# Performance work log

Measured on AMD Instinct MI355X. Metric: run time of the kernel, lower is better.

Reference implementation:

```python
import jax, jax.numpy as jnp
import numpy as np

# scNET (vae_flag=False, cd=False, eval mode): genes x cells matrix;
# PPI graph over 3000 genes, KNN graph over 4096 cells.
N_GENES, N_CELLS = 3000, 4096          # col_dim, row_dim
INTER_R, EMBD_R = 512, 128             # gene (rows) encoder dims
INTER_C, EMBD_C = 1024, 256            # cell (cols) encoder dims
N_LAYERS = 2
KNN_E, PPI_E = 65536, 262144
SCALE_PARAM = 3.0                      # TransformerConvReducrLayer scale_param


def setup_inputs() -> dict:
    key = jax.random.key(0)
    ks = iter(jax.random.split(key, 64))
    def lin(shape):
        fan_in = shape[-2]
        return jax.random.normal(next(ks), shape, jnp.float32) / np.sqrt(fan_in)
    inp = {}
    inp["x"] = jax.random.normal(next(ks), (N_GENES, N_CELLS), jnp.float32)
    inp["knn_ei"] = jax.random.randint(next(ks), (2, KNN_E), 0, N_CELLS)
    inp["ppi_ei"] = jax.random.randint(next(ks), (2, PPI_E), 0, N_GENES)
    inp["rl_W"] = lin((N_CELLS, N_CELLS)); inp["rl_b"] = jnp.zeros((N_CELLS,), jnp.float32)
    inp["rs_Wl"] = lin((N_LAYERS, N_CELLS, N_CELLS)); inp["rs_Wr"] = lin((N_LAYERS, N_CELLS, N_CELLS))
    inp["rs_b"] = jnp.zeros((N_LAYERS, N_CELLS), jnp.float32)
    inp["cs_Wl"] = lin((N_LAYERS, N_GENES, N_GENES)); inp["cs_Wr"] = lin((N_LAYERS, N_GENES, N_GENES))
    inp["cs_b"] = jnp.zeros((N_LAYERS, N_GENES), jnp.float32)
    inp["rg_W"] = lin((N_CELLS, INTER_R)); inp["rg_b"] = jnp.zeros((INTER_R,), jnp.float32)
    for nm in ("rq", "rk", "rv", "rsk"):
        inp[nm + "_W"] = lin((INTER_R, EMBD_R)); inp[nm + "_b"] = jnp.zeros((EMBD_R,), jnp.float32)
    inp["cg_W"] = lin((N_GENES, INTER_C)); inp["cg_b"] = jnp.zeros((INTER_C,), jnp.float32)
    for nm in ("cq", "ck", "cv", "csk"):
        inp[nm + "_W"] = lin((INTER_C, EMBD_C)); inp[nm + "_b"] = jnp.zeros((EMBD_C,), jnp.float32)
    inp["d1_W"] = lin((EMBD_C, INTER_C)); inp["d1_b"] = jnp.zeros((INTER_C,), jnp.float32)
    inp["d2_W"] = lin((INTER_C, INTER_C)); inp["d2_b"] = jnp.zeros((INTER_C,), jnp.float32)
    inp["d3_W"] = lin((INTER_C, N_GENES)); inp["d3_b"] = jnp.zeros((N_GENES,), jnp.float32)
    return inp


def sage_conv(x, ei, Wl, Wr, b):
    # PyG SAGEConv (mean aggr, root weight): lin_l(mean_{j->i} x_j) + lin_r(x_i) + b
    n = x.shape[0]
    src, dst = ei[0], ei[1]
    s = jax.ops.segment_sum(x[src], dst, num_segments=n)
    cnt = jax.ops.segment_sum(jnp.ones((ei.shape[1],), x.dtype), dst, num_segments=n)
    agg = s / jnp.maximum(cnt, 1.0)[:, None]
    return agg @ Wl + x @ Wr + b


def gcn_conv(x, ei, W, b):
    # PyG GCNConv: self loops + symmetric D^-1/2 (A+I) D^-1/2 normalization
    n = x.shape[0]
    idx = jnp.arange(n)
    src = jnp.concatenate([ei[0], idx])
    dst = jnp.concatenate([ei[1], idx])
    deg = jax.ops.segment_sum(jnp.ones((src.shape[0],), x.dtype), dst, num_segments=n)
    dinv = jax.lax.rsqrt(jnp.maximum(deg, 1.0))
    h = x @ W
    msg = h[src] * (dinv[src] * dinv[dst])[:, None]
    return jax.ops.segment_sum(msg, dst, num_segments=n) + b


def transformer_conv(x, ei, Wq, bq, Wk, bk, Wv, bv, Ws, bs, scale_param):
    # PyG TransformerConv (heads=1). scale_param=None -> per-destination segment
    # softmax; otherwise scNET's globally sigmoid-normalized attention
    # (TransformerConvReducrLayer.message): global mean/std standardize -> sigmoid.
    n = x.shape[0]
    d = Wq.shape[1]
    src, dst = ei[0], ei[1]
    q = x @ Wq + bq
    k = x @ Wk + bk
    v = x @ Wv + bv
    alpha = (q[dst] * k[src]).sum(-1) / jnp.sqrt(jnp.asarray(d, x.dtype))  # [E]
    if scale_param is None:
        m = jax.ops.segment_max(alpha, dst, num_segments=n)
        e = jnp.exp(alpha - m[dst])
        z = jax.ops.segment_sum(e, dst, num_segments=n)
        alpha = e / (z[dst] + 1e-16)
    else:
        alpha = (alpha - alpha.mean()) / ((1.0 / scale_param) * jnp.std(alpha, ddof=1))
        alpha = jax.nn.sigmoid(alpha)
    out = jax.ops.segment_sum(v[src] * alpha[:, None], dst, num_segments=n)
    return out + (x @ Ws + bs)  # root skip (lin_skip)


def reference(x, knn_ei, ppi_ei, rl_W, rl_b, rs_Wl, rs_Wr, rs_b, cs_Wl, cs_Wr, cs_b,
              rg_W, rg_b, rq_W, rq_b, rk_W, rk_b, rv_W, rv_b, rsk_W, rsk_b,
              cg_W, cg_b, cq_W, cq_b, ck_W, ck_b, cv_W, cv_b, csk_W, csk_b,
              d1_W, d1_b, d2_W, d2_b, d3_W, d3_b):
    # MutaelEncoder: row linear then alternating col/row SAGE layers (dropout=id in eval)
    h = x @ rl_W + rl_b                                   # [G, C]
    for i in range(N_LAYERS):
        h = jax.nn.leaky_relu(sage_conv(h.T, knn_ei, cs_Wl[i], cs_Wr[i], cs_b[i]), 0.01).T
        h = jax.nn.leaky_relu(sage_conv(h, ppi_ei, rs_Wl[i], rs_Wr[i], rs_b[i]), 0.01)
    # rows (gene) DimEncoder: GCN -> LeakyReLU -> TransformerConv (softmax attention)
    r = jax.nn.leaky_relu(gcn_conv(h, ppi_ei, rg_W, rg_b), 0.01)
    row_embed = transformer_conv(r, ppi_ei, rq_W, rq_b, rk_W, rk_b, rv_W, rv_b, rsk_W, rsk_b, None)
    # cols (cell) DimEncoder (reducer): GCN -> LeakyReLU -> sigmoid-normalized attention
    c = jax.nn.leaky_relu(gcn_conv(h.T, knn_ei, cg_W, cg_b), 0.01)
    col_embed = transformer_conv(c, knn_ei, cq_W, cq_b, ck_W, ck_b, cv_W, cv_b, csk_W, csk_b, SCALE_PARAM)
    # FatureDecoder (cd=False): 3-layer MLP with ReLU (dropout=id in eval)
    d = jax.nn.relu(col_embed @ d1_W + d1_b)
    d = jax.nn.relu(d @ d2_W + d2_b)
    recon = d @ d3_W + d3_b                               # [C_cells, G]
    return row_embed, col_embed, recon
```

## Files before the change

### kernel.cpp

```cpp
#include <hip/hip_runtime.h>
#include <math.h>

#define N_GENES 3000
#define N_CELLS 4096
#define GPAD    3072
#define INTER_R 512
#define EMBD_R  128
#define INTER_C 1024
#define EMBD_C  256
#define KNN_E   65536
#define PPI_E   262144

typedef unsigned short u16;
typedef __bf16 bf16x8 __attribute__((ext_vector_type(8)));
typedef float f32x4 __attribute__((ext_vector_type(4)));

__device__ __forceinline__ float b2f(u16 u) {
  union { unsigned i; float f; } x; x.i = ((unsigned)u) << 16; return x.f;
}
__device__ __forceinline__ u16 f2b(float f) {
  union { float f; unsigned i; } x; x.f = f;
  unsigned r = (x.i + 0x7FFFu + ((x.i >> 16) & 1u)) >> 16;
  return (u16)r;
}

typedef const void __attribute__((address_space(1))) gvoid;
typedef void __attribute__((address_space(3))) svoid;
__device__ __forceinline__ void gload16(const void* g, void* l) {
  __builtin_amdgcn_global_load_lds((gvoid*)g, (svoid*)l, 16, 0, 0);
}

template <int OUTF32, int MF>
__global__ __launch_bounds__(512, 1) void mgemm8_k(
    const u16* __restrict__ A, int lda, const u16* __restrict__ BT, int ldb,
    const float* __restrict__ bias, int biasRow, void* __restrict__ Cv, int ldc,
    int M, int N, int K, int accum, int act, int nbx) {
  constexpr int MFH = MF / 2;
  constexpr int TM = MF * 32;
  constexpr int ABYTES = TM * 64;
  constexpr int BBYTES = 16384;
  constexpr int BUFB = 2 * ABYTES + 2 * BBYTES;
  __shared__ char S[2 * BUFB];
  const int t = threadIdx.x;
  const int wid = t >> 6;
  const int l = t & 63;
  const int wm = wid >> 2, wn = wid & 3;
  const int fr = l & 15, hi = l >> 4;

  int nwg = gridDim.x, bid = blockIdx.x;
  int q = nwg >> 3, r = nwg & 7, xcd = bid & 7, seq = bid >> 3;
  int sid = (xcd < r ? xcd * (q + 1) : r * (q + 1) + (xcd - r) * q) + seq;
  int by = sid / nbx, bx = sid - by * nbx;
  const int row0 = by * TM, col0 = bx * 256;

  f32x4 acc[MF][4];
#pragma unroll
  for (int i = 0; i < MF; i++)
#pragma unroll
    for (int j = 0; j < 4; j++) acc[i][j] = (f32x4){0.f, 0.f, 0.f, 0.f};

  const int cA1 = t, cA2 = t + 512;
  const int rA1 = cA1 >> 2, rA2 = cA2 >> 2;
  const int gA1 = (cA1 & 3) ^ ((rA1 >> 1) & 3);
  const int gA2 = (cA2 & 3) ^ ((rA2 >> 1) & 3);
  int arow1 = row0 + rA1; arow1 = arow1 < M ? arow1 : M - 1;
  int arow2 = row0 + (rA2 < TM ? rA2 : TM - 1); arow2 = arow2 < M ? arow2 : M - 1;
  const u16* baseA1 = A + (size_t)arow1 * lda + gA1 * 8;
  const u16* baseA2 = A + (size_t)arow2 * lda + gA2 * 8;
  const bool doA2 = (MF == 8) || (t < 256);
  int brow1 = col0 + rA1; brow1 = brow1 < N ? brow1 : N - 1;
  int brow2 = col0 + rA2; brow2 = brow2 < N ? brow2 : N - 1;
  const u16* baseB1 = BT + (size_t)brow1 * ldb + gA1 * 8;
  const u16* baseB2 = BT + (size_t)brow2 * ldb + gA2 * 8;

  auto aoff = [](int buf, int kh) { return buf * BUFB + kh * ABYTES; };
  auto boff = [](int buf, int kh) { return buf * BUFB + 2 * ABYTES + kh * BBYTES; };

  auto stageA = [&](int buf, int kh, int kt) {
    int ko = kt * 64 + kh * 32;
    gload16(baseA1 + ko, S + aoff(buf, kh) + cA1 * 16);
    if (doA2) gload16(baseA2 + ko, S + aoff(buf, kh) + cA2 * 16);
  };
  auto stageB = [&](int buf, int kh, int kt) {
    int ko = kt * 64 + kh * 32;
    gload16(baseB1 + ko, S + boff(buf, kh) + cA1 * 16);
    gload16(baseB2 + ko, S + boff(buf, kh) + cA2 * 16);
  };

  bf16x8 af[MFH], bfr[4];
  auto dsrA = [&](int buf, int kh, int mh) {
#pragma unroll
    for (int i = 0; i < MFH; i++) {
      int row = wm * (MF * 16) + (mh * MFH + i) * 16 + fr;
      af[i] = *(const bf16x8*)(S + aoff(buf, kh) + row * 64 +
                               ((hi ^ ((row >> 1) & 3)) << 4));
    }
  };
  auto dsrB = [&](int buf, int kh) {
#pragma unroll
    for (int i = 0; i < 4; i++) {
      int row = wn * 64 + i * 16 + fr;
      bfr[i] = *(const bf16x8*)(S + boff(buf, kh) + row * 64 +
                                ((hi ^ ((row >> 1) & 3)) << 4));
    }
  };
  auto mma = [&](int mh) {
    __builtin_amdgcn_s_setprio(1);
#pragma unroll
    for (int i = 0; i < MFH; i++)
#pragma unroll
      for (int j = 0; j < 4; j++)
        acc[mh * MFH + i][j] = __builtin_amdgcn_mfma_f32_16x16x32_bf16(
            af[i], bfr[j], acc[mh * MFH + i][j], 0, 0, 0);
    __builtin_amdgcn_s_setprio(0);
  };
  auto vmw = [&]() {
    if (MF == 6 && wid >= 4)
      asm volatile("s_waitcnt vmcnt(4)" ::: "memory");
    else
      asm volatile("s_waitcnt vmcnt(6)" ::: "memory");
  };
  auto barmid = [&]() {
    __builtin_amdgcn_sched_barrier(0);
    __builtin_amdgcn_s_barrier();
    asm volatile("s_waitcnt lgkmcnt(0)" ::: "memory");
    __builtin_amdgcn_sched_barrier(0);
  };
  auto barend = [&]() {
    __builtin_amdgcn_sched_barrier(0);
    __builtin_amdgcn_s_barrier();
    __builtin_amdgcn_sched_barrier(0);
  };

  const int nt = K >> 6;
  stageA(0, 0, 0); stageB(0, 0, 0); stageA(0, 1, 0); stageB(0, 1, 0);
  stageA(1, 0, 1); stageB(1, 0, 1); stageA(1, 1, 1);
  vmw();
  __builtin_amdgcn_sched_barrier(0);
  __builtin_amdgcn_s_barrier();
  __builtin_amdgcn_sched_barrier(0);

  int p = 0;
  for (int kt = 0; kt < nt - 2; kt++, p ^= 1) {
    dsrA(p, 0, 0); dsrB(p, 0);
    stageB(p ^ 1, 1, kt + 1);
    barmid(); mma(0); barend();
    dsrA(p, 0, 1);
    stageA(p, 0, kt + 2);
    barmid(); mma(1); barend();
    dsrA(p, 1, 0); dsrB(p, 1);
    stageB(p, 0, kt + 2);
    barmid(); mma(0); barend();
    dsrA(p, 1, 1);
    stageA(p, 1, kt + 2);
    vmw();
    barmid(); mma(1); barend();
  }
  dsrA(p, 0, 0); dsrB(p, 0);
  stageB(p ^ 1, 1, nt - 1);
  barmid(); mma(0); barend();
  dsrA(p, 0, 1);
  barmid(); mma(1); barend();
  dsrA(p, 1, 0); dsrB(p, 1);
  barmid(); mma(0); barend();
  dsrA(p, 1, 1);
  asm volatile("s_waitcnt vmcnt(0)" ::: "memory");
  barmid(); mma(1); barend();
  p ^= 1;
  dsrA(p, 0, 0); dsrB(p, 0);
  barmid(); mma(0); barend();
  dsrA(p, 0, 1);
  barmid(); mma(1); barend();
  dsrA(p, 1, 0); dsrB(p, 1);
  barmid(); mma(0); barend();
  dsrA(p, 1, 1);
  barmid(); mma(1); barend();

#pragma unroll
  for (int mf = 0; mf < MF; mf++) {
    int mb = row0 + wm * (MF * 16) + mf * 16 + hi * 4;
#pragma unroll
    for (int rr2 = 0; rr2 < 4; rr2++) {
      int m = mb + rr2;
      if (m >= M) continue;
#pragma unroll
      for (int nf = 0; nf < 4; nf++) {
        int n = col0 + wn * 64 + nf * 16 + fr;
        if (n >= N) continue;
        float v = acc[mf][nf][rr2];
        if (bias) v += biasRow ? bias[m] : bias[n];
        if (OUTF32) {
          float* C = (float*)Cv;
          if (accum) v += C[(size_t)m * ldc + n];
          if (act == 1) v = v > 0.f ? v : 0.01f * v;
          else if (act == 2) v = fmaxf(v, 0.f);
          C[(size_t)m * ldc + n] = v;
        } else {
          u16* C = (u16*)Cv;
          if (accum) v += b2f(C[(size_t)m * ldc + n]);
          if (act == 1) v = v > 0.f ? v : 0.01f * v;
          else if (act == 2) v = fmaxf(v, 0.f);
          C[(size_t)m * ldc + n] = f2b(v);
        }
      }
    }
  }
}

template <int OUTF32>
__global__ __launch_bounds__(256) void mgemm_k(
    const u16* __restrict__ A, int lda, const u16* __restrict__ BT, int ldb,
    const float* __restrict__ bias, void* __restrict__ Cv, int ldc,
    int M, int N, int K, int accum, int act, int nbx) {
  __shared__ u16 As[2][64 * 64];
  __shared__ u16 Bs[2][64 * 64];
  const int t = threadIdx.x;
  const int w = t >> 6, l = t & 63;
  const int wr = w >> 1, wc = w & 1;
  const int fr = l & 15, hi = l >> 4;

  int nwg = gridDim.x, bid = blockIdx.x;
  int q = nwg >> 3, r = nwg & 7, xcd = bid & 7, seq = bid >> 3;
  int sid = (xcd < r ? xcd * (q + 1) : r * (q + 1) + (xcd - r) * q) + seq;
  int by = sid / nbx, bx = sid - by * nbx;
  const int row0 = by * 128, col0 = bx * 128;

  f32x4 acc[4][4];
#pragma unroll
  for (int i = 0; i < 4; i++)
#pragma unroll
    for (int j = 0; j < 4; j++) acc[i][j] = (f32x4){0.f, 0.f, 0.f, 0.f};

  const u16* Aad[2]; const u16* Bad[2];
  char* Alds[2]; char* Blds[2];
#pragma unroll
  for (int c = 0; c < 2; c++) {
    int P = (w * 2 + c) * 64 + l;
    int prow = P >> 3, s = P & 7;
    int lr = prow * 2 + (s >> 2);
    int g = (s & 3) ^ (prow & 3);
    int ar = row0 + lr; ar = ar < M ? ar : M - 1;
    int br = col0 + lr; br = br < N ? br : N - 1;
    Aad[c] = A + (size_t)ar * lda + g * 8;
    Bad[c] = BT + (size_t)br * ldb + g * 8;
    Alds[c] = (char*)&As[0][0] + P * 16;
    Blds[c] = (char*)&Bs[0][0] + P * 16;
  }
  const int nt = K >> 5;
  auto stage = [&](int tt, int b) {
    int ko = tt << 5;
#pragma unroll
    for (int c = 0; c < 2; c++) {
      gload16(Aad[c] + ko, Alds[c] + b * 8192);
      gload16(Bad[c] + ko, Blds[c] + b * 8192);
    }
  };
  auto compute = [&](int tt) {
    const u16* Ab = As[tt & 1];
    const u16* Bb = Bs[tt & 1];
    bf16x8 af[4], bfr[4];
#pragma unroll
    for (int mi = 0; mi < 4; mi++) {
      int row = wr * 64 + mi * 16 + fr;
      int pr = row >> 1;
      af[mi] = *(const bf16x8*)&Ab[pr * 64 + ((row & 1) * 4 + (hi ^ (pr & 3))) * 8];
    }
#pragma unroll
    for (int ni = 0; ni < 4; ni++) {
      int row = wc * 64 + ni * 16 + fr;
      int pr = row >> 1;
      bfr[ni] = *(const bf16x8*)&Bb[pr * 64 + ((row & 1) * 4 + (hi ^ (pr & 3))) * 8];
    }
    __builtin_amdgcn_s_setprio(1);
#pragma unroll
    for (int mi = 0; mi < 4; mi++)
#pragma unroll
      for (int ni = 0; ni < 4; ni++)
        acc[mi][ni] = __builtin_amdgcn_mfma_f32_16x16x32_bf16(
            af[mi], bfr[ni], acc[mi][ni], 0, 0, 0);
    __builtin_amdgcn_s_setprio(0);
  };

  stage(0, 0);
  if (nt > 1) stage(1, 1);
  for (int tt = 0; tt < nt - 1; tt++) {
    asm volatile("s_waitcnt vmcnt(4)" ::: "memory");
    __builtin_amdgcn_sched_barrier(0);
    __builtin_amdgcn_s_barrier();
    __builtin_amdgcn_sched_barrier(0);
    compute(tt);
    __builtin_amdgcn_sched_barrier(0);
    __builtin_amdgcn_s_barrier();
    __builtin_amdgcn_sched_barrier(0);
    if (tt + 2 < nt) stage(tt + 2, tt & 1);
  }
  asm volatile("s_waitcnt vmcnt(0)" ::: "memory");
  __builtin_amdgcn_sched_barrier(0);
  __builtin_amdgcn_s_barrier();
  __builtin_amdgcn_sched_barrier(0);
  compute(nt - 1);

#pragma unroll
  for (int mi = 0; mi < 4; mi++) {
    int mb = row0 + wr * 64 + mi * 16 + hi * 4;
#pragma unroll
    for (int rr2 = 0; rr2 < 4; rr2++) {
      int m = mb + rr2;
      if (m >= M) continue;
#pragma unroll
      for (int ni = 0; ni < 4; ni++) {
        int n = col0 + wc * 64 + ni * 16 + fr;
        if (n >= N) continue;
        float v = acc[mi][ni][rr2];
        if (bias) v += bias[n];
        if (OUTF32) {
          float* C = (float*)Cv;
          if (accum) v += C[(size_t)m * ldc + n];
          if (act == 1) v = v > 0.f ? v : 0.01f * v;
          else if (act == 2) v = fmaxf(v, 0.f);
          C[(size_t)m * ldc + n] = v;
        } else {
          u16* C = (u16*)Cv;
          if (accum) v += b2f(C[(size_t)m * ldc + n]);
          if (act == 1) v = v > 0.f ? v : 0.01f * v;
          else if (act == 2) v = fmaxf(v, 0.f);
          C[(size_t)m * ldc + n] = f2b(v);
        }
      }
    }
  }
}

__global__ void cvtw_k(const float* __restrict__ in, int K, int Nw,
                       u16* __restrict__ out, int ldb, int Kpad) {
  __shared__ float tile[32][33];
  int k0 = blockIdx.y * 32, n0 = blockIdx.x * 32;
  int tx = threadIdx.x & 31, ty = threadIdx.x >> 5;
  for (int i = ty; i < 32; i += 8)
    tile[i][tx] = (k0 + i < K && n0 + tx < Nw) ? in[(size_t)(k0 + i) * Nw + n0 + tx] : 0.f;
  __syncthreads();
  for (int i = ty; i < 32; i += 8) {
    int n = n0 + i, k = k0 + tx;
    if (n < Nw && k < Kpad) out[(size_t)n * ldb + k] = f2b(tile[tx][i]);
  }
}

__global__ void tpad_k(const u16* __restrict__ in, int R, int C, int lin,
                       u16* __restrict__ out, int ostride, int Rpad) {
  __shared__ u16 tile[32][33];
  int r0 = blockIdx.y * 32, c0 = blockIdx.x * 32;
  int tx = threadIdx.x & 31, ty = threadIdx.x >> 5;
  for (int i = ty; i < 32; i += 8)
    tile[i][tx] = (r0 + i < R && c0 + tx < C) ? in[(size_t)(r0 + i) * lin + c0 + tx] : (u16)0;
  __syncthreads();
  for (int i = ty; i < 32; i += 8) {
    int c = c0 + i, r = r0 + tx;
    if (c < C && r < Rpad) out[(size_t)c * ostride + r] = tile[tx][i];
  }
}

__global__ void cvtx_k(const float* __restrict__ in, u16* __restrict__ out, int n) {
  int i = (blockIdx.x * 256 + threadIdx.x) * 4;
  if (i >= n) return;
  float4 v = *(const float4*)&in[i];
  uint2 o;
  o.x = (unsigned)f2b(v.x) | ((unsigned)f2b(v.y) << 16);
  o.y = (unsigned)f2b(v.z) | ((unsigned)f2b(v.w) << 16);
  *(uint2*)&out[i] = o;
}

__global__ void catbias_k(const float* b0, const float* b1, const float* b2,
                          const float* b3, int seg, float* out) {
  int i = blockIdx.x * 256 + threadIdx.x;
  if (i >= 4 * seg) return;
  const float* s = i < seg ? b0 : i < 2 * seg ? b1 : i < 3 * seg ? b2 : b3;
  out[i] = s[i & (seg - 1)];
}

__global__ void zero_i32(int* __restrict__ p, int n) {
  int i = blockIdx.x * 256 + threadIdx.x;
  if (i < n) p[i] = 0;
}
__global__ void count_k(const int* __restrict__ dst, int E, int* __restrict__ cnt) {
  int e = blockIdx.x * 256 + threadIdx.x;
  if (e < E) atomicAdd(&cnt[dst[e]], 1);
}
__global__ __launch_bounds__(1024) void scan_k(const int* __restrict__ cnt,
                                               int* __restrict__ rs, int N) {
  __shared__ int sd[1024];
  int t = threadIdx.x;
  int per = (N + 1023) >> 10;
  int base = t * per;
  int loc[4];
  int s = 0;
  for (int u = 0; u < per; u++) {
    int idx = base + u;
    loc[u] = s;
    int v = (idx < N) ? cnt[idx] : 0;
    s += v;
  }
  sd[t] = s;
  __syncthreads();
  for (int off = 1; off < 1024; off <<= 1) {
    int v = (t >= off) ? sd[t - off] : 0;
    __syncthreads();
    sd[t] += v;
    __syncthreads();
  }
  int prev = (t > 0) ? sd[t - 1] : 0;
  for (int u = 0; u < per; u++) {
    int idx = base + u;
    if (idx < N) rs[idx] = prev + loc[u];
  }
  if (t == 0) rs[N] = sd[1023];
}
__global__ void fill_k(const int* __restrict__ src, const int* __restrict__ dst, int E,
                       const int* __restrict__ rs, int* cursor,
                       int* __restrict__ csrc, int* __restrict__ ceid) {
  int e = blockIdx.x * 256 + threadIdx.x;
  if (e >= E) return;
  int d = dst[e];
  int p = atomicAdd(&cursor[d], 1);
  int b = rs[d] + p;
  csrc[b] = src[e];
  ceid[b] = e;
}
__global__ void dinv_k(const int* __restrict__ rs, float* __restrict__ dinv, int N) {
  int i = blockIdx.x * 256 + threadIdx.x;
  if (i < N) dinv[i] = rsqrtf((float)(rs[i + 1] - rs[i] + 1));
}

__global__ void sage_agg_k(const u16* __restrict__ X, int ld, const int* __restrict__ rs,
                           const int* __restrict__ csrc, u16* __restrict__ out, int D) {
  int i = blockIdx.y;
  int j8 = (blockIdx.x * 256 + threadIdx.x) * 8;
  if (j8 >= D) return;
  int s = rs[i], e = rs[i + 1];
  float a[8] = {0, 0, 0, 0, 0, 0, 0, 0};
  for (int p = s; p < e; p++) {
    uint4 v = *(const uint4*)&X[(size_t)csrc[p] * ld + j8];
    a[0] += b2f(v.x & 0xffff); a[1] += b2f(v.x >> 16);
    a[2] += b2f(v.y & 0xffff); a[3] += b2f(v.y >> 16);
    a[4] += b2f(v.z & 0xffff); a[5] += b2f(v.z >> 16);
    a[6] += b2f(v.w & 0xffff); a[7] += b2f(v.w >> 16);
  }
  float inv = 1.f / fmaxf((float)(e - s), 1.f);
  uint4 o;
  o.x = (unsigned)f2b(a[0] * inv) | ((unsigned)f2b(a[1] * inv) << 16);
  o.y = (unsigned)f2b(a[2] * inv) | ((unsigned)f2b(a[3] * inv) << 16);
  o.z = (unsigned)f2b(a[4] * inv) | ((unsigned)f2b(a[5] * inv) << 16);
  o.w = (unsigned)f2b(a[6] * inv) | ((unsigned)f2b(a[7] * inv) << 16);
  *(uint4*)&out[(size_t)i * ld + j8] = o;
}

__global__ void gcn_agg_k(const u16* __restrict__ HW, int ld, const int* __restrict__ rs,
                          const int* __restrict__ csrc, const float* __restrict__ dinv,
                          const float* __restrict__ bias, u16* __restrict__ out, int D) {
  int i = blockIdx.y;
  int j8 = (blockIdx.x * 256 + threadIdx.x) * 8;
  if (j8 >= D) return;
  int s = rs[i], e = rs[i + 1];
  float a[8] = {0, 0, 0, 0, 0, 0, 0, 0};
  for (int p = s; p < e; p++) {
    int sr = csrc[p];
    float w = dinv[sr];
    uint4 v = *(const uint4*)&HW[(size_t)sr * ld + j8];
    a[0] += b2f(v.x & 0xffff) * w; a[1] += b2f(v.x >> 16) * w;
    a[2] += b2f(v.y & 0xffff) * w; a[3] += b2f(v.y >> 16) * w;
    a[4] += b2f(v.z & 0xffff) * w; a[5] += b2f(v.z >> 16) * w;
    a[6] += b2f(v.w & 0xffff) * w; a[7] += b2f(v.w >> 16) * w;
  }
  float di = dinv[i];
  uint4 sv = *(const uint4*)&HW[(size_t)i * ld + j8];
  float sf[8] = {b2f(sv.x & 0xffff), b2f(sv.x >> 16), b2f(sv.y & 0xffff), b2f(sv.y >> 16),
                 b2f(sv.z & 0xffff), b2f(sv.z >> 16), b2f(sv.w & 0xffff), b2f(sv.w >> 16)};
  unsigned o[4];
#pragma unroll
  for (int qq = 0; qq < 4; qq++) {
    float v0 = di * a[2 * qq] + sf[2 * qq] * di * di + bias[j8 + 2 * qq];
    float v1 = di * a[2 * qq + 1] + sf[2 * qq + 1] * di * di + bias[j8 + 2 * qq + 1];
    v0 = v0 > 0.f ? v0 : 0.01f * v0;
    v1 = v1 > 0.f ? v1 : 0.01f * v1;
    o[qq] = (unsigned)f2b(v0) | ((unsigned)f2b(v1) << 16);
  }
  *(uint4*)&out[(size_t)i * ld + j8] = *(uint4*)o;
}

__global__ void attn_row_k(const u16* __restrict__ QKVS, const int* __restrict__ rs,
                           const int* __restrict__ csrc, float* __restrict__ out, int N) {
  int node = blockIdx.x * 4 + (threadIdx.x >> 6);
  if (node >= N) return;
  int lane = threadIdx.x & 63;
  const u16* base = QKVS + (size_t)node * 512;
  unsigned qb = *(const unsigned*)&base[lane * 2];
  float qx = b2f(qb & 0xffff), qy = b2f(qb >> 16);
  int s = rs[node], e = rs[node + 1];
  float m = -1e30f, z = 0.f, ax = 0.f, ay = 0.f;
  const float scale = 0.08838834764831845f;
  for (int p = s; p < e; p++) {
    const u16* kb = QKVS + (size_t)csrc[p] * 512;
    unsigned kw = *(const unsigned*)&kb[128 + lane * 2];
    float part = qx * b2f(kw & 0xffff) + qy * b2f(kw >> 16);
#pragma unroll
    for (int off = 32; off; off >>= 1) part += __shfl_xor(part, off);
    float a = part * scale;
    float mn = fmaxf(m, a);
    float sc = __expf(m - mn);
    float wv = __expf(a - mn);
    z = z * sc + wv;
    unsigned vw = *(const unsigned*)&kb[256 + lane * 2];
    ax = ax * sc + wv * b2f(vw & 0xffff);
    ay = ay * sc + wv * b2f(vw >> 16);
    m = mn;
  }
  float inv = (e == s) ? 0.f : 1.f / (z + 1e-16f);
  unsigned sw = *(const unsigned*)&base[384 + lane * 2];
  out[(size_t)node * 128 + lane * 2] = ax * inv + b2f(sw & 0xffff);
  out[(size_t)node * 128 + lane * 2 + 1] = ay * inv + b2f(sw >> 16);
}

__global__ void col_alpha_k(const u16* __restrict__ QKVS, const int* __restrict__ src,
                            const int* __restrict__ dst, float* __restrict__ alpha, int E) {
  int e = blockIdx.x * 4 + (threadIdx.x >> 6);
  if (e >= E) return;
  int lane = threadIdx.x & 63;
  uint2 qb = *(const uint2*)&QKVS[(size_t)dst[e] * 1024 + lane * 4];
  uint2 kb = *(const uint2*)&QKVS[(size_t)src[e] * 1024 + 256 + lane * 4];
  float p = b2f(qb.x & 0xffff) * b2f(kb.x & 0xffff) + b2f(qb.x >> 16) * b2f(kb.x >> 16) +
            b2f(qb.y & 0xffff) * b2f(kb.y & 0xffff) + b2f(qb.y >> 16) * b2f(kb.y >> 16);
#pragma unroll
  for (int off = 32; off; off >>= 1) p += __shfl_xor(p, off);
  if (lane == 0) alpha[e] = p * 0.0625f;
}

__global__ void stats_k(const float* __restrict__ alpha, int E, double* __restrict__ st) {
  __shared__ double s1[256], s2[256];
  int t = threadIdx.x;
  double a1 = 0, a2 = 0;
  for (int i = blockIdx.x * 256 + t; i < E; i += gridDim.x * 256) {
    double a = alpha[i];
    a1 += a; a2 += a * a;
  }
  s1[t] = a1; s2[t] = a2;
  __syncthreads();
  for (int off = 128; off; off >>= 1) {
    if (t < off) { s1[t] += s1[t + off]; s2[t] += s2[t + off]; }
    __syncthreads();
  }
  if (t == 0) { atomicAdd(&st[0], s1[0]); atomicAdd(&st[1], s2[0]); }
}

__global__ void col_attn_agg_k(const u16* __restrict__ QKVS, const float* __restrict__ alpha,
                               const int* __restrict__ rs, const int* __restrict__ csrc,
                               const int* __restrict__ ceid, const double* __restrict__ st,
                               float* __restrict__ outf, u16* __restrict__ outb, int E) {
  int i = blockIdx.x;
  int j = threadIdx.x;
  double mean = st[0] / E;
  double var = (st[1] - E * mean * mean) / (double)(E - 1);
  float rstd = (float)(1.0 / sqrt(var));
  float fm = (float)mean;
  int s = rs[i], e = rs[i + 1];
  float acc = 0.f;
  for (int p = s; p < e; p++) {
    float a = alpha[ceid[p]];
    float x = 3.0f * (a - fm) * rstd;
    float sg = 1.f / (1.f + __expf(-x));
    acc += sg * b2f(QKVS[(size_t)csrc[p] * 1024 + 512 + j]);
  }
  float res = acc + b2f(QKVS[(size_t)i * 1024 + 768 + j]);
  outf[(size_t)i * 256 + j] = res;
  outb[(size_t)i * 256 + j] = f2b(res);
}

extern "C" void kernel_launch(void* const* d_in, const int* in_sizes, int n_in,
                              void* d_out, int out_size, void* d_ws, size_t ws_size,
                              hipStream_t stream) {
  const float* x      = (const float*)d_in[0];
  const int*   knn_ei = (const int*)d_in[1];
  const int*   ppi_ei = (const int*)d_in[2];
  const float* rl_W   = (const float*)d_in[3];
  const float* rl_b   = (const float*)d_in[4];
  const float* rs_Wl  = (const float*)d_in[5];
  const float* rs_Wr  = (const float*)d_in[6];
  const float* rs_b   = (const float*)d_in[7];
  const float* cs_Wl  = (const float*)d_in[8];
  const float* cs_Wr  = (const float*)d_in[9];
  const float* cs_b   = (const float*)d_in[10];
  const float* rg_W   = (const float*)d_in[11];
  const float* rg_b   = (const float*)d_in[12];
  const float* rq_W   = (const float*)d_in[13];
  const float* rq_b   = (const float*)d_in[14];
  const float* rk_W   = (const float*)d_in[15];
  const float* rk_b   = (const float*)d_in[16];
  const float* rv_W   = (const float*)d_in[17];
  const float* rv_b   = (const float*)d_in[18];
  const float* rsk_W  = (const float*)d_in[19];
  const float* rsk_b  = (const float*)d_in[20];
  const float* cg_W   = (const float*)d_in[21];
  const float* cg_b   = (const float*)d_in[22];
  const float* cq_W   = (const float*)d_in[23];
  const float* cq_b   = (const float*)d_in[24];
  const float* ck_W   = (const float*)d_in[25];
  const float* ck_b   = (const float*)d_in[26];
  const float* cv_W   = (const float*)d_in[27];
  const float* cv_b   = (const float*)d_in[28];
  const float* csk_W  = (const float*)d_in[29];
  const float* csk_b  = (const float*)d_in[30];
  const float* d1_W   = (const float*)d_in[31];
  const float* d1_b   = (const float*)d_in[32];
  const float* d2_W   = (const float*)d_in[33];
  const float* d2_b   = (const float*)d_in[34];
  const float* d3_W   = (const float*)d_in[35];
  const float* d3_b   = (const float*)d_in[36];
  float* out = (float*)d_out;

  char* ws = (char*)d_ws;
  size_t off = 0;
  auto alloc = [&](size_t bytes) -> void* {
    void* p = ws + off;
    off = (off + bytes + 255) & ~(size_t)255;
    return p;
  };
  u16* P0 = (u16*)alloc((size_t)N_GENES * N_CELLS * 2);
  u16* P1 = (u16*)alloc((size_t)N_CELLS * GPAD * 2);
  u16* P2 = (u16*)alloc((size_t)N_CELLS * GPAD * 2);
  u16* CR = (u16*)alloc((size_t)N_CELLS * 2 * GPAD * 2);
  u16* BTs = (u16*)alloc((size_t)N_CELLS * 2 * N_CELLS * 2);
  u16* CEb = (u16*)alloc((size_t)N_CELLS * EMBD_C * 2);
  float* catb = (float*)alloc(1024 * 4);
  int* knn_rs  = (int*)alloc((N_CELLS + 1) * 4);
  int* knn_cnt = (int*)alloc(N_CELLS * 4);
  int* knn_cur = (int*)alloc(N_CELLS * 4);
  int* knn_src = (int*)alloc(KNN_E * 4);
  int* knn_eid = (int*)alloc(KNN_E * 4);
  int* ppi_rs  = (int*)alloc((N_GENES + 1) * 4);
  int* ppi_cnt = (int*)alloc(N_GENES * 4);
  int* ppi_cur = (int*)alloc(N_GENES * 4);
  int* ppi_src = (int*)alloc(PPI_E * 4);
  int* ppi_eid = (int*)alloc(PPI_E * 4);
  float* dinv_knn = (float*)alloc(N_CELLS * 4);
  float* dinv_ppi = (float*)alloc(N_GENES * 4);
  float* alphaB   = (float*)alloc(KNN_E * 4);
  double* stats   = (double*)alloc(2 * 8);
  u16* xb = CR;
  u16* RA = CR;
  u16* CA = P1;

  auto cvtw = [&](const float* W, int K, int Nw, u16* dst, int ldb, int Kpad) {
    dim3 g((Nw + 31) / 32, (Kpad + 31) / 32);
    cvtw_k<<<g, 256, 0, stream>>>(W, K, Nw, dst, ldb, Kpad);
  };
  auto mg = [&](const u16* A, int lda, const u16* BT, int ldb, const float* bias,
                void* C, int ldc, int M, int N, int K, int accum, int act, int outf32) {
    int nbx = (N + 127) / 128, nby = (M + 127) / 128;
    dim3 g(nbx * nby);
    if (outf32)
      mgemm_k<1><<<g, 256, 0, stream>>>(A, lda, BT, ldb, bias, C, ldc, M, N, K, accum, act, nbx);
    else
      mgemm_k<0><<<g, 256, 0, stream>>>(A, lda, BT, ldb, bias, C, ldc, M, N, K, accum, act, nbx);
  };
  auto mg8 = [&](const u16* A, int lda, const u16* BT, int ldb, const float* bias,
                 int biasRow, void* C, int ldc, int M, int N, int K, int act, int outf32) {
    int nbx = (N + 255) / 256, nby = (M + 191) / 192;
    dim3 g(nbx * nby);
    if (outf32)
      mgemm8_k<1, 6><<<g, 512, 0, stream>>>(A, lda, BT, ldb, bias, biasRow, C, ldc,
                                            M, N, K, 0, act, nbx);
    else
      mgemm8_k<0, 6><<<g, 512, 0, stream>>>(A, lda, BT, ldb, bias, biasRow, C, ldc,
                                            M, N, K, 0, act, nbx);
  };
  auto tpad = [&](const u16* in, int R, int C, int lin, u16* o, int ostride, int Rpad) {
    dim3 g((C + 31) / 32, (Rpad + 31) / 32);
    tpad_k<<<g, 256, 0, stream>>>(in, R, C, lin, o, ostride, Rpad);
  };
  auto sage = [&](const u16* X, int ld, const int* rs, const int* csrc, u16* o,
                  int nodes, int D) {
    dim3 g((D / 8 + 255) / 256, nodes);
    sage_agg_k<<<g, 256, 0, stream>>>(X, ld, rs, csrc, o, D);
  };
  auto gcn = [&](const u16* HW, int ld, const int* rs, const int* csrc, const float* dinv,
                 const float* bias, u16* o, int nodes, int D) {
    dim3 g((D / 8 + 255) / 256, nodes);
    gcn_agg_k<<<g, 256, 0, stream>>>(HW, ld, rs, csrc, dinv, bias, o, D);
  };

  zero_i32<<<(N_CELLS + 255) / 256, 256, 0, stream>>>(knn_cnt, N_CELLS);
  count_k<<<(KNN_E + 255) / 256, 256, 0, stream>>>(knn_ei + KNN_E, KNN_E, knn_cnt);
  scan_k<<<1, 1024, 0, stream>>>(knn_cnt, knn_rs, N_CELLS);
  zero_i32<<<(N_CELLS + 255) / 256, 256, 0, stream>>>(knn_cur, N_CELLS);
  fill_k<<<(KNN_E + 255) / 256, 256, 0, stream>>>(knn_ei, knn_ei + KNN_E, KNN_E,
                                                  knn_rs, knn_cur, knn_src, knn_eid);
  dinv_k<<<(N_CELLS + 255) / 256, 256, 0, stream>>>(knn_rs, dinv_knn, N_CELLS);
  zero_i32<<<(N_GENES + 255) / 256, 256, 0, stream>>>(ppi_cnt, N_GENES);
  count_k<<<(PPI_E + 255) / 256, 256, 0, stream>>>(ppi_ei + PPI_E, PPI_E, ppi_cnt);
  scan_k<<<1, 1024, 0, stream>>>(ppi_cnt, ppi_rs, N_GENES);
  zero_i32<<<(N_GENES + 255) / 256, 256, 0, stream>>>(ppi_cur, N_GENES);
  fill_k<<<(PPI_E + 255) / 256, 256, 0, stream>>>(ppi_ei, ppi_ei + PPI_E, PPI_E,
                                                  ppi_rs, ppi_cur, ppi_src, ppi_eid);
  dinv_k<<<(N_GENES + 255) / 256, 256, 0, stream>>>(ppi_rs, dinv_ppi, N_GENES);

  cvtx_k<<<(N_GENES * N_CELLS / 4 + 255) / 256, 256, 0, stream>>>(
      x, xb, N_GENES * N_CELLS);
  cvtw(rl_W, N_CELLS, N_CELLS, BTs, N_CELLS, N_CELLS);
  mg8(xb, N_CELLS, BTs, N_CELLS, rl_b, 0, P0, N_CELLS, N_GENES, N_CELLS, N_CELLS, 0, 0);

  for (int i = 0; i < 2; i++) {
    const float* cWl = cs_Wl + (size_t)i * N_GENES * N_GENES;
    const float* cWr = cs_Wr + (size_t)i * N_GENES * N_GENES;
    const float* cb  = cs_b + (size_t)i * N_GENES;
    const float* rWl = rs_Wl + (size_t)i * N_CELLS * N_CELLS;
    const float* rWr = rs_Wr + (size_t)i * N_CELLS * N_CELLS;
    const float* rb  = rs_b + (size_t)i * N_CELLS;
    tpad(P0, N_GENES, N_CELLS, N_CELLS, CA + GPAD, 2 * GPAD, GPAD);
    sage(CA + GPAD, 2 * GPAD, knn_rs, knn_src, CA, N_CELLS, GPAD);
    cvtw(cWl, N_GENES, N_GENES, BTs, 2 * GPAD, GPAD);
    cvtw(cWr, N_GENES, N_GENES, BTs + GPAD, 2 * GPAD, GPAD);
    mg8(BTs, 2 * GPAD, CA, 2 * GPAD, cb, 1, RA + N_CELLS, 2 * N_CELLS,
        N_GENES, N_CELLS, 2 * GPAD, 1, 0);
    sage(RA + N_CELLS, 2 * N_CELLS, ppi_rs, ppi_src, RA, N_GENES, N_CELLS);
    cvtw(rWl, N_CELLS, N_CELLS, BTs, 2 * N_CELLS, N_CELLS);
    cvtw(rWr, N_CELLS, N_CELLS, BTs + N_CELLS, 2 * N_CELLS, N_CELLS);
    mg8(RA, 2 * N_CELLS, BTs, 2 * N_CELLS, rb, 0, P0, N_CELLS,
        N_GENES, N_CELLS, 2 * N_CELLS, 1, 0);
  }

  cvtw(rg_W, N_CELLS, INTER_R, BTs, N_CELLS, N_CELLS);
  mg(P0, N_CELLS, BTs, N_CELLS, nullptr, P1, INTER_R, N_GENES, INTER_R, N_CELLS, 0, 0, 0);
  gcn(P1, INTER_R, ppi_rs, ppi_src, dinv_ppi, rg_b, P2, N_GENES, INTER_R);
  cvtw(rq_W, INTER_R, EMBD_R, BTs + (size_t)0 * EMBD_R * INTER_R, INTER_R, INTER_R);
  cvtw(rk_W, INTER_R, EMBD_R, BTs + (size_t)1 * EMBD_R * INTER_R, INTER_R, INTER_R);
  cvtw(rv_W, INTER_R, EMBD_R, BTs + (size_t)2 * EMBD_R * INTER_R, INTER_R, INTER_R);
  cvtw(rsk_W, INTER_R, EMBD_R, BTs + (size_t)3 * EMBD_R * INTER_R, INTER_R, INTER_R);
  catbias_k<<<2, 256, 0, stream>>>(rq_b, rk_b, rv_b, rsk_b, EMBD_R, catb);
  mg(P2, INTER_R, BTs, INTER_R, catb, P1, 4 * EMBD_R, N_GENES, 4 * EMBD_R, INTER_R, 0, 0, 0);
  attn_row_k<<<(N_GENES + 3) / 4, 256, 0, stream>>>(P1, ppi_rs, ppi_src, out, N_GENES);

  tpad(P0, N_GENES, N_CELLS, N_CELLS, P1, GPAD, GPAD);
  cvtw(cg_W, N_GENES, INTER_C, BTs, GPAD, GPAD);
  mg(P1, GPAD, BTs, GPAD, nullptr, P2, INTER_C, N_CELLS, INTER_C, GPAD, 0, 0, 0);
  gcn(P2, INTER_C, knn_rs, knn_src, dinv_knn, cg_b, P0, N_CELLS, INTER_C);
  cvtw(cq_W, INTER_C, EMBD_C, BTs + (size_t)0 * EMBD_C * INTER_C, INTER_C, INTER_C);
  cvtw(ck_W, INTER_C, EMBD_C, BTs + (size_t)1 * EMBD_C * INTER_C, INTER_C, INTER_C);
  cvtw(cv_W, INTER_C, EMBD_C, BTs + (size_t)2 * EMBD_C * INTER_C, INTER_C, INTER_C);
  cvtw(csk_W, INTER_C, EMBD_C, BTs + (size_t)3 * EMBD_C * INTER_C, INTER_C, INTER_C);
  catbias_k<<<4, 256, 0, stream>>>(cq_b, ck_b, cv_b, csk_b, EMBD_C, catb);
  mg(P0, INTER_C, BTs, INTER_C, catb, P1, 4 * EMBD_C, N_CELLS, 4 * EMBD_C, INTER_C, 0, 0, 0);
  col_alpha_k<<<KNN_E / 4, 256, 0, stream>>>(P1, knn_ei, knn_ei + KNN_E, alphaB, KNN_E);
  zero_i32<<<1, 256, 0, stream>>>((int*)stats, 4);
  stats_k<<<64, 256, 0, stream>>>(alphaB, KNN_E, stats);
  float* col_embed = out + (size_t)N_GENES * EMBD_R;
  col_attn_agg_k<<<N_CELLS, 256, 0, stream>>>(P1, alphaB, knn_rs, knn_src, knn_eid,
                                              stats, col_embed, CEb, KNN_E);

  u16* D1 = CR;
  u16* D2 = CR + (size_t)N_CELLS * INTER_C;
  float* recon = col_embed + (size_t)N_CELLS * EMBD_C;
  cvtw(d1_W, EMBD_C, INTER_C, BTs, EMBD_C, EMBD_C);
  mg(CEb, EMBD_C, BTs, EMBD_C, d1_b, D1, INTER_C, N_CELLS, INTER_C, EMBD_C, 0, 2, 0);
  cvtw(d2_W, INTER_C, INTER_C, BTs, INTER_C, INTER_C);
  mg(D1, INTER_C, BTs, INTER_C, d2_b, D2, INTER_C, N_CELLS, INTER_C, INTER_C, 0, 2, 0);
  cvtw(d3_W, INTER_C, N_GENES, BTs, INTER_C, INTER_C);
  mg(D2, INTER_C, BTs, INTER_C, d3_b, recon, N_GENES, N_CELLS, N_GENES, INTER_C, 0, 0, 1);
}
```

Measured before the change: 2.256 ms.

## Tile SAGE aggregation into column slabs and remap GEMM tiles per XCD

The SAGE mean aggregation now runs as a series of launches, one per 512-column slab. Each wavefront handles one node and each block covers four nodes. The intent is to keep the gathered source-row slices of each slab resident in L2 across nodes, instead of streaming full-width rows. Separately, when the block-row count is a multiple of eight, the GEMM block-to-tile mapping assigns whole block rows to each XCD so that XCD's L2 can reuse the A tile. The cost is more kernel launches, and the wave-per-node mapping may load-imbalance across nodes of different degree.

New measurement: 2.516 ms. +11.5%, slower.

```diff
diff --git a/kernel.cpp b/kernel.cpp
--- a/kernel.cpp
+++ b/kernel.cpp
@@ -48,16 +48,25 @@
   const int fr = l & 15, hi = l >> 4;
 
   int nwg = gridDim.x, bid = blockIdx.x;
-  int q = nwg >> 3, r = nwg & 7, xcd = bid & 7, seq = bid >> 3;
-  int sid = (xcd < r ? xcd * (q + 1) : r * (q + 1) + (xcd - r) * q) + seq;
-  int by = sid / nbx, bx = sid - by * nbx;
+  int nby = nwg / nbx;
+  int xcd = bid & 7, j = bid >> 3;
+  int by, bx;
+  if ((nby & 7) == 0 && (nwg & 7) == 0) {
+    int pass = j / nbx;
+    bx = j - pass * nbx;
+    by = xcd + 8 * pass;
+  } else {
+    int q = nwg >> 3, r = nwg & 7;
+    int sid = (xcd < r ? xcd * (q + 1) : r * (q + 1) + (xcd - r) * q) + j;
+    by = sid / nbx; bx = sid - by * nbx;
+  }
   const int row0 = by * TM, col0 = bx * 256;
 
   f32x4 acc[MF][4];
 #pragma unroll
   for (int i = 0; i < MF; i++)
 #pragma unroll
-    for (int j = 0; j < 4; j++) acc[i][j] = (f32x4){0.f, 0.f, 0.f, 0.f};
+    for (int jj = 0; jj < 4; jj++) acc[i][jj] = (f32x4){0.f, 0.f, 0.f, 0.f};
 
   const int cA1 = t, cA2 = t + 512;
   const int rA1 = cA1 >> 2, rA2 = cA2 >> 2;
@@ -109,9 +118,9 @@
 #pragma unroll
     for (int i = 0; i < MFH; i++)
 #pragma unroll
-      for (int j = 0; j < 4; j++)
-        acc[mh * MFH + i][j] = __builtin_amdgcn_mfma_f32_16x16x32_bf16(
-            af[i], bfr[j], acc[mh * MFH + i][j], 0, 0, 0);
+      for (int jj = 0; jj < 4; jj++)
+        acc[mh * MFH + i][jj] = __builtin_amdgcn_mfma_f32_16x16x32_bf16(
+            af[i], bfr[jj], acc[mh * MFH + i][jj], 0, 0, 0);
     __builtin_amdgcn_s_setprio(0);
   };
   auto vmw = [&]() {
@@ -229,7 +238,7 @@
 #pragma unroll
   for (int i = 0; i < 4; i++)
 #pragma unroll
-    for (int j = 0; j < 4; j++) acc[i][j] = (f32x4){0.f, 0.f, 0.f, 0.f};
+    for (int jj = 0; jj < 4; jj++) acc[i][jj] = (f32x4){0.f, 0.f, 0.f, 0.f};
 
   const u16* Aad[2]; const u16* Bad[2];
   char* Alds[2]; char* Blds[2];
@@ -430,12 +439,13 @@
   if (i < N) dinv[i] = rsqrtf((float)(rs[i + 1] - rs[i] + 1));
 }
 
-__global__ void sage_agg_k(const u16* __restrict__ X, int ld, const int* __restrict__ rs,
-                           const int* __restrict__ csrc, u16* __restrict__ out, int D) {
-  int i = blockIdx.y;
-  int j8 = (blockIdx.x * 256 + threadIdx.x) * 8;
-  if (j8 >= D) return;
-  int s = rs[i], e = rs[i + 1];
+__global__ void sage_slab_k(const u16* __restrict__ X, int ld, const int* __restrict__ rs,
+                            const int* __restrict__ csrc, u16* __restrict__ out,
+                            int nodes, int Doff) {
+  int node = blockIdx.x * 4 + (threadIdx.x >> 6);
+  if (node >= nodes) return;
+  int j8 = Doff + (threadIdx.x & 63) * 8;
+  int s = rs[node], e = rs[node + 1];
   float a[8] = {0, 0, 0, 0, 0, 0, 0, 0};
   for (int p = s; p < e; p++) {
     uint4 v = *(const uint4*)&X[(size_t)csrc[p] * ld + j8];
@@ -450,7 +460,7 @@
   o.y = (unsigned)f2b(a[2] * inv) | ((unsigned)f2b(a[3] * inv) << 16);
   o.z = (unsigned)f2b(a[4] * inv) | ((unsigned)f2b(a[5] * inv) << 16);
   o.w = (unsigned)f2b(a[6] * inv) | ((unsigned)f2b(a[7] * inv) << 16);
-  *(uint4*)&out[(size_t)i * ld + j8] = o;
+  *(uint4*)&out[(size_t)node * ld + j8] = o;
 }
 
 __global__ void gcn_agg_k(const u16* __restrict__ HW, int ld, const int* __restrict__ rs,
@@ -677,8 +687,9 @@
   };
   auto sage = [&](const u16* X, int ld, const int* rs, const int* csrc, u16* o,
                   int nodes, int D) {
-    dim3 g((D / 8 + 255) / 256, nodes);
-    sage_agg_k<<<g, 256, 0, stream>>>(X, ld, rs, csrc, o, D);
+    int nb = (nodes + 3) / 4;
+    for (int s = 0; s < D; s += 512)
+      sage_slab_k<<<nb, 256, 0, stream>>>(X, ld, rs, csrc, o, nodes, s);
   };
   auto gcn = [&](const u16* HW, int ld, const int* rs, const int* csrc, const float* dinv,
                  const float* bias, u16* o, int nodes, int D) {
```
